# Optimization experiments

Hardware: AMD Instinct MI355X
Metric: run time of the kernel (lower is better)

The kernel has to match this reference:

```python
import math
import jax, jax.numpy as jnp
import numpy as np

L, H, C, T = 6, 16, 1024, 256   # layers, heads, n_embd, context steps (seq = 3T)
NACT, D_FF, B = 80, 4096, 4

def _conv(x, w, b, s, p):
    y = jax.lax.conv_general_dilated(x, w, (s, s), [(p, p), (p, p)],
                                     dimension_numbers=('NCHW', 'OIHW', 'NCHW'))
    return y + b[None, :, None, None]

def _ln(x, g, b):
    m = x.mean(-1, keepdims=True)
    v = ((x - m) ** 2).mean(-1, keepdims=True)
    return (x - m) / jnp.sqrt(v + 1e-5) * g + b

def _forward(states, rtgs, meta_states, circuit_feas,
             conv1_w, conv1_b, conv2_w, conv2_b, conv3_w, conv3_b,
             enc_w, enc_b, meta_w1, meta_b1, meta_w2, meta_b2,
             ret_w, ret_b, act_emb, pos_emb, gpos_emb,
             ln1_g, ln1_b, ln2_g, ln2_b,
             Wq, bq, Wk, bk, Wv, bv, Wo, bo,
             Wm1, bm1, Wm2, bm2, lnf_g, lnf_b, head_w,
             actions, timesteps):
    Bb, Tl = states.shape[0], states.shape[1]
    # state CNN encoder: (B*T, 8, 8, 10) -> 16 feats -> Linear(16, C-4)
    s = states.reshape(-1, 8, 8, 10)
    h = jax.nn.relu(_conv(s, conv1_w, conv1_b, 2, 1))
    h = jax.nn.relu(_conv(h, conv2_w, conv2_b, 2, 1))
    h = jax.nn.relu(_conv(h, conv3_w, conv3_b, 2, 1))
    se = h.reshape(h.shape[0], -1) @ enc_w + enc_b                    # (B*T, C-4)
    me = jax.nn.relu(meta_states.reshape(-1, 4) @ meta_w1 + meta_b1) @ meta_w2 + meta_b2
    state_emb = jnp.tanh(jnp.concatenate([se, me], axis=1)).reshape(Bb, Tl, C)
    # circuit embedding is computed then zeroed in source (no_circuit_emb=True) -> no effect
    rtg_emb = jnp.tanh(rtgs @ ret_w + ret_b)                          # (B, T, C)
    act_e = act_emb[actions[..., 0]]                                  # (B, T, C)
    # interleave (rtg, state, action) per timestep -> (B, 3T, C)
    tok = jnp.stack([rtg_emb, state_emb, act_e], axis=2).reshape(Bb, 3 * Tl, C)
    pos = gpos_emb[0, timesteps[:, 0, 0]][:, None, :] + pos_emb[:, :3 * Tl, :]
    x = tok + pos
    mask = jnp.tril(jnp.ones((3 * Tl, 3 * Tl), bool))
    d = C // H
    for i in range(L):
        hx = _ln(x, ln1_g[i], ln1_b[i])
        q = (hx @ Wq[i] + bq[i]).reshape(Bb, 3 * Tl, H, d)
        k = (hx @ Wk[i] + bk[i]).reshape(Bb, 3 * Tl, H, d)
        v = (hx @ Wv[i] + bv[i]).reshape(Bb, 3 * Tl, H, d)
        att = jnp.einsum('bqhd,bkhd->bhqk', q, k) / math.sqrt(d)
        att = jax.nn.softmax(jnp.where(mask, att, -jnp.inf), axis=-1)
        y = jnp.einsum('bhqk,bkhd->bqhd', att, v).reshape(Bb, 3 * Tl, C)
        x = x + (y @ Wo[i] + bo[i])
        h2 = _ln(x, ln2_g[i], ln2_b[i])
        x = x + (jax.nn.gelu(h2 @ Wm1[i] + bm1[i], approximate=False) @ Wm2[i] + bm2[i])
    logits = _ln(x, lnf_g, lnf_b) @ head_w                            # (B, 3T, NACT)
    return logits[:, 1::3, :]                                         # predictions at state tokens

def setup_inputs():
    ks = iter(jax.random.split(jax.random.key(0), 64))
    def W(*shape):
        return jax.random.normal(next(ks), shape, jnp.float32) * 0.02
    return {
        'states': jax.random.normal(next(ks), (B, T, 640), jnp.float32),
        'rtgs': jax.random.normal(next(ks), (B, T, 1), jnp.float32),
        'meta_states': jax.random.normal(next(ks), (B, T, 4), jnp.float32),
        'circuit_feas': jax.random.normal(next(ks), (B, 768), jnp.float32),
        'conv1_w': W(16, 8, 8, 8), 'conv1_b': jnp.zeros(16),
        'conv2_w': W(32, 16, 4, 4), 'conv2_b': jnp.zeros(32),
        'conv3_w': W(16, 32, 3, 3), 'conv3_b': jnp.zeros(16),
        'enc_w': W(16, C - 4), 'enc_b': jnp.zeros(C - 4),
        'meta_w1': W(4, 32), 'meta_b1': jnp.zeros(32),
        'meta_w2': W(32, 4), 'meta_b2': jnp.zeros(4),
        'ret_w': W(1, C), 'ret_b': jnp.zeros(C),
        'act_emb': W(NACT, C),
        'pos_emb': W(1, 3 * T + 1, C), 'gpos_emb': W(1, T + 1, C),
        'ln1_g': jnp.ones((L, C)), 'ln1_b': jnp.zeros((L, C)),
        'ln2_g': jnp.ones((L, C)), 'ln2_b': jnp.zeros((L, C)),
        'Wq': W(L, C, C), 'bq': jnp.zeros((L, C)),
        'Wk': W(L, C, C), 'bk': jnp.zeros((L, C)),
        'Wv': W(L, C, C), 'bv': jnp.zeros((L, C)),
        'Wo': W(L, C, C), 'bo': jnp.zeros((L, C)),
        'Wm1': W(L, C, D_FF), 'bm1': jnp.zeros((L, D_FF)),
        'Wm2': W(L, D_FF, C), 'bm2': jnp.zeros((L, C)),
        'lnf_g': jnp.ones(C), 'lnf_b': jnp.zeros(C),
        'head_w': W(C, NACT),
        'actions': jax.random.randint(next(ks), (B, T, 1), 0, NACT),
        'timesteps': jax.random.randint(next(ks), (B, 1, 1), 0, T + 1),
    }

def reference(states, rtgs, meta_states, circuit_feas,
              conv1_w, conv1_b, conv2_w, conv2_b, conv3_w, conv3_b,
              enc_w, enc_b, meta_w1, meta_b1, meta_w2, meta_b2,
              ret_w, ret_b, act_emb, pos_emb, gpos_emb,
              ln1_g, ln1_b, ln2_g, ln2_b,
              Wq, bq, Wk, bk, Wv, bv, Wo, bo,
              Wm1, bm1, Wm2, bm2, lnf_g, lnf_b, head_w,
              actions, timesteps):
    return _forward(states, rtgs, meta_states, circuit_feas,
                    conv1_w, conv1_b, conv2_w, conv2_b, conv3_w, conv3_b,
                    enc_w, enc_b, meta_w1, meta_b1, meta_w2, meta_b2,
                    ret_w, ret_b, act_emb, pos_emb, gpos_emb,
                    ln1_g, ln1_b, ln2_g, ln2_b,
                    Wq, bq, Wk, bk, Wv, bv, Wo, bo,
                    Wm1, bm1, Wm2, bm2, lnf_g, lnf_b, head_w,
                    actions, timesteps)
```

## Files before the change

### kernel.cpp

```cpp
#include <hip/hip_runtime.h>
#include <hip/hip_bf16.h>


#define S_LEN 768
#define C_DIM 1024
#define NHEAD 16
#define HDIM 64
#define BATCH 4
#define TCTX 256
#define DFF 4096
#define NACT 80
#define MROWS (BATCH * S_LEN)

typedef __attribute__((ext_vector_type(4))) float f32x4;
typedef __attribute__((ext_vector_type(8))) short bf16x8;
typedef __attribute__((ext_vector_type(8))) _Float16 f16x8;

static __device__ __forceinline__ unsigned short f2bf(float f) {
    unsigned int u = __float_as_uint(f);
    u += 0x7FFF + ((u >> 16) & 1);
    return (unsigned short)(u >> 16);
}
static __device__ __forceinline__ float bf2f(unsigned short h) {
    return __uint_as_float(((unsigned int)h) << 16);
}
static __device__ __forceinline__ unsigned short f2h(float f) {
    _Float16 h = (_Float16)f;
    return __builtin_bit_cast(unsigned short, h);
}

static __device__ __forceinline__ void gload16(void* l, const void* g) {
    __builtin_amdgcn_global_load_lds(
        (__attribute__((address_space(1))) void*)(g),
        (__attribute__((address_space(3))) void*)(l), 16, 0, 0);
}

__global__ __launch_bounds__(256) void transpose_w_kernel(
    const float* __restrict__ Wq, const float* __restrict__ Wk,
    const float* __restrict__ Wv, const float* __restrict__ Wo,
    const float* __restrict__ Wm1, const float* __restrict__ Wm2,
    unsigned short* __restrict__ Wb)
{
    const int t = blockIdx.x;
    const float* src; unsigned short* dst; int K, N, kt, nt;
    if (t < 1024) {
        const int m = t >> 8, tile = t & 255;
        src = (m == 0) ? Wq : (m == 1) ? Wk : (m == 2) ? Wv : Wo;
        dst = Wb + (size_t)m * 1048576;
        K = 1024; N = 1024; kt = tile >> 4; nt = tile & 15;
    } else if (t < 2048) {
        const int tile = t - 1024;
        src = Wm1; dst = Wb + (size_t)4 * 1048576;
        K = 1024; N = 4096; kt = tile >> 6; nt = tile & 63;
    } else {
        const int tile = t - 2048;
        src = Wm2; dst = Wb + (size_t)8 * 1048576;
        K = 4096; N = 1024; kt = tile >> 4; nt = tile & 15;
    }
    const int k0 = kt * 64, n0 = nt * 64;
    __shared__ float Ls[64][65];

    const int r = threadIdx.x >> 2, p = threadIdx.x & 3;
    #pragma unroll
    for (int i = 0; i < 4; ++i)
        *(float4*)&Ls[r][p * 16 + i * 4] =
            *(const float4*)&src[(size_t)(k0 + r) * N + n0 + p * 16 + i * 4];
    __syncthreads();

    unsigned short __align__(16) h[16];
    #pragma unroll
    for (int i = 0; i < 16; ++i) h[i] = f2bf(Ls[p * 16 + i][r]);
    unsigned short* d = dst + (size_t)(n0 + r) * K + k0 + p * 16;
    *(uint4*)d       = *(uint4*)&h[0];
    *(uint4*)(d + 8) = *(uint4*)&h[8];
}

__global__ __launch_bounds__(256) void embed_kernel(
    const float* __restrict__ states, const float* __restrict__ rtgs,
    const float* __restrict__ meta,
    const float* __restrict__ c1w, const float* __restrict__ c1b,
    const float* __restrict__ c2w, const float* __restrict__ c2b,
    const float* __restrict__ c3w, const float* __restrict__ c3b,
    const float* __restrict__ encw, const float* __restrict__ encb,
    const float* __restrict__ mw1, const float* __restrict__ mb1,
    const float* __restrict__ mw2, const float* __restrict__ mb2,
    const float* __restrict__ retw, const float* __restrict__ retb,
    const float* __restrict__ aemb, const float* __restrict__ pos,
    const float* __restrict__ gpos,
    const int* __restrict__ actions, const int* __restrict__ timesteps,
    float* __restrict__ X)
{
    const int n = blockIdx.x;
    const int b = n >> 8, t = n & 255;
    const int tid = threadIdx.x;

    __shared__ float sin_[640];
    __shared__ float h1[96];
    __shared__ float h2[32];
    __shared__ float feat[16];
    __shared__ float hidm[32];
    __shared__ float mer[4];

    for (int e = tid; e < 640; e += 256)
        sin_[e] = states[(size_t)n * 640 + e];
    __syncthreads();

    if (tid < 96) {
        int o = tid / 6, rem = tid % 6, oh = rem / 3, ow = rem % 3;
        float a = c1b[o];
        for (int ci = 0; ci < 8; ++ci)
            for (int kh = 0; kh < 8; ++kh) {
                int ih = oh * 2 - 1 + kh;
                if (ih < 0 || ih >= 8) continue;
                for (int kw = 0; kw < 8; ++kw) {
                    int iw = ow * 2 - 1 + kw;
                    if (iw < 0 || iw >= 10) continue;
                    a += c1w[((o * 8 + ci) * 8 + kh) * 8 + kw] * sin_[ci * 80 + ih * 10 + iw];
                }
            }
        h1[tid] = fmaxf(a, 0.f);
    }
    if (tid < 32) {
        float a = mb1[tid];
        for (int i = 0; i < 4; ++i)
            a += meta[(size_t)n * 4 + i] * mw1[i * 32 + tid];
        hidm[tid] = fmaxf(a, 0.f);
    }
    __syncthreads();

    if (tid < 32) {
        float a = c2b[tid];
        for (int ci = 0; ci < 16; ++ci)
            for (int kh = 0; kh < 4; ++kh) {
                int ih = -1 + kh;
                if (ih < 0 || ih >= 2) continue;
                for (int kw = 0; kw < 4; ++kw) {
                    int iw = -1 + kw;
                    if (iw < 0 || iw >= 3) continue;
                    a += c2w[((tid * 16 + ci) * 4 + kh) * 4 + kw] * h1[ci * 6 + ih * 3 + iw];
                }
            }
        h2[tid] = fmaxf(a, 0.f);
    }
    __syncthreads();

    if (tid < 16) {
        float a = c3b[tid];
        for (int ci = 0; ci < 32; ++ci)
            a += c3w[(tid * 32 + ci) * 9 + 4] * h2[ci];
        feat[tid] = fmaxf(a, 0.f);
    }
    if (tid < 4) {
        float a = mb2[tid];
        for (int j = 0; j < 32; ++j) a += hidm[j] * mw2[j * 4 + tid];
        mer[tid] = a;
    }
    __syncthreads();

    const float r = rtgs[n];
    const int a_idx = actions[n];
    const int g = timesteps[b];
    const size_t xbase = ((size_t)b * S_LEN + 3 * t) * C_DIM;

    for (int c = tid; c < C_DIM; c += 256) {
        float se;
        if (c < 1020) {
            float acc = encb[c];
            #pragma unroll
            for (int k = 0; k < 16; ++k) acc += feat[k] * encw[k * 1020 + c];
            se = acc;
        } else {
            se = mer[c - 1020];
        }
        const float st = tanhf(se);
        const float rt = tanhf(r * retw[c] + retb[c]);
        const float ae = aemb[(size_t)a_idx * C_DIM + c];
        const float gp = gpos[(size_t)g * C_DIM + c];
        X[xbase + c]             = rt + gp + pos[(size_t)(3 * t + 0) * C_DIM + c];
        X[xbase + C_DIM + c]     = st + gp + pos[(size_t)(3 * t + 1) * C_DIM + c];
        X[xbase + 2 * C_DIM + c] = ae + gp + pos[(size_t)(3 * t + 2) * C_DIM + c];
    }
}

__global__ __launch_bounds__(256) void ln_bf16_kernel(
    const float* __restrict__ in, unsigned short* __restrict__ out,
    const float* __restrict__ gw, const float* __restrict__ bw)
{
    const int row = blockIdx.x * 4 + (threadIdx.x >> 6);
    const int lane = threadIdx.x & 63;
    const float* x = in + (size_t)row * C_DIM;

    float4 v[4];
    float s = 0.f;
    #pragma unroll
    for (int j = 0; j < 4; ++j) {
        v[j] = *(const float4*)&x[lane * 4 + j * 256];
        s += (v[j].x + v[j].y) + (v[j].z + v[j].w);
    }
    #pragma unroll
    for (int o = 1; o < 64; o <<= 1) s += __shfl_xor(s, o, 64);
    const float mean = s * (1.0f / 1024.0f);

    float s2 = 0.f;
    #pragma unroll
    for (int j = 0; j < 4; ++j) {
        float dx = v[j].x - mean, dy = v[j].y - mean;
        float dz = v[j].z - mean, dw = v[j].w - mean;
        s2 += (dx * dx + dy * dy) + (dz * dz + dw * dw);
    }
    #pragma unroll
    for (int o = 1; o < 64; o <<= 1) s2 += __shfl_xor(s2, o, 64);
    const float inv = rsqrtf(s2 * (1.0f / 1024.0f) + 1e-5f);

    #pragma unroll
    for (int j = 0; j < 4; ++j) {
        const int c = lane * 4 + j * 256;
        ushort4 o4;
        o4.x = f2bf((v[j].x - mean) * inv * gw[c + 0] + bw[c + 0]);
        o4.y = f2bf((v[j].y - mean) * inv * gw[c + 1] + bw[c + 1]);
        o4.z = f2bf((v[j].z - mean) * inv * gw[c + 2] + bw[c + 2]);
        o4.w = f2bf((v[j].w - mean) * inv * gw[c + 3] + bw[c + 3]);
        *(ushort4*)&out[(size_t)row * C_DIM + c] = o4;
    }
}

__device__ __forceinline__ void gemm_core(
    const unsigned short* __restrict__ A, const unsigned short* __restrict__ Bt,
    int row0, int col0, int ldk, int nk, f32x4 (&acc)[4][4])
{
    __shared__ __align__(16) unsigned short As[3][4][128][8];
    __shared__ __align__(16) unsigned short Bs[3][4][128][8];

    const int tid = threadIdx.x;
    const int ar  = tid & 63, akg = tid >> 6;
    const int lane = tid & 63, w = tid >> 6;
    const int rwl = (w >> 1) * 64, cwl = (w & 1) * 64;
    const int mi = lane & 15, kg = lane >> 4;

    const unsigned short* pa = A + (size_t)(row0 + ar) * ldk + akg * 8;
    const unsigned short* pb = Bt + (size_t)(col0 + ar) * ldk + akg * 8;
    const size_t rstep = (size_t)64 * ldk;

    gload16(&As[0][akg][ar][0],      pa);
    gload16(&As[0][akg][ar + 64][0], pa + rstep);
    gload16(&Bs[0][akg][ar][0],      pb);
    gload16(&Bs[0][akg][ar + 64][0], pb + rstep);
    gload16(&As[1][akg][ar][0],      pa + 32);
    gload16(&As[1][akg][ar + 64][0], pa + rstep + 32);
    gload16(&Bs[1][akg][ar][0],      pb + 32);
    gload16(&Bs[1][akg][ar + 64][0], pb + rstep + 32);

#define GEMM_STEP(CB, PB, KK, VM)                                          \
    {                                                                      \
        asm volatile("s_waitcnt vmcnt(" #VM ")" ::: "memory");             \
        __builtin_amdgcn_s_barrier();                                      \
        __builtin_amdgcn_sched_barrier(0);                                 \
        if ((KK) + 2 < nk) {                                               \
            const unsigned short* ga = pa + (size_t)((KK) + 2) * 32;       \
            const unsigned short* gb = pb + (size_t)((KK) + 2) * 32;       \
            gload16(&As[PB][akg][ar][0],      ga);                         \
            gload16(&As[PB][akg][ar + 64][0], ga + rstep);                 \
            gload16(&Bs[PB][akg][ar][0],      gb);                         \
            gload16(&Bs[PB][akg][ar + 64][0], gb + rstep);                 \
        }                                                                  \
        bf16x8 af[4], bfr[4];                                              \
        _Pragma("unroll")                                                  \
        for (int i = 0; i < 4; ++i) {                                      \
            af[i]  = *(const bf16x8*)&As[CB][kg][rwl + i * 16 + mi][0];    \
            bfr[i] = *(const bf16x8*)&Bs[CB][kg][cwl + i * 16 + mi][0];    \
        }                                                                  \
        __builtin_amdgcn_s_setprio(1);                                     \
        _Pragma("unroll")                                                  \
        for (int ri = 0; ri < 4; ++ri)                                     \
            _Pragma("unroll")                                              \
            for (int ci = 0; ci < 4; ++ci)                                 \
                acc[ri][ci] = __builtin_amdgcn_mfma_f32_16x16x32_bf16(     \
                    af[ri], bfr[ci], acc[ri][ci], 0, 0, 0);                \
        __builtin_amdgcn_s_setprio(0);                                     \
    }

    int k = 0;
    while (k + 4 < nk) {
        GEMM_STEP(0, 2, k,     4)
        GEMM_STEP(1, 0, k + 1, 4)
        GEMM_STEP(2, 1, k + 2, 4)
        k += 3;
    }
    GEMM_STEP(0, 2, k,     4)
    GEMM_STEP(1, 0, k + 1, 0)
#undef GEMM_STEP
}

template<int ACT, int OUTB, int RES>
__global__ __launch_bounds__(256) void mfma_gemm(
    const unsigned short* __restrict__ A, const unsigned short* __restrict__ Bt,
    const float* __restrict__ bias, const float* resid,
    float* outf, unsigned short* __restrict__ outb,
    int N, int K)
{
    const int row0 = blockIdx.y * 128, col0 = blockIdx.x * 128;
    f32x4 acc[4][4] = {};
    gemm_core(A, Bt, row0, col0, K, K >> 5, acc);

    const int lane = threadIdx.x & 63, w = threadIdx.x >> 6;
    const int rwl = (w >> 1) * 64, cwl = (w & 1) * 64;
    const int mi = lane & 15, kg = lane >> 4;

    #pragma unroll
    for (int ri = 0; ri < 4; ++ri) {
        #pragma unroll
        for (int ci = 0; ci < 4; ++ci) {
            #pragma unroll
            for (int j = 0; j < 4; ++j) {
                const int row = row0 + rwl + ri * 16 + kg * 4 + j;
                const int col = col0 + cwl + ci * 16 + mi;
                float v = acc[ri][ci][j] + bias[col];
                if (ACT) v = 0.5f * v * (1.0f + erff(v * 0.70710678118f));
                if (RES) v += resid[(size_t)row * N + col];
                if (OUTB) outb[(size_t)row * N + col] = f2bf(v);
                else      outf[(size_t)row * N + col] = v;
            }
        }
    }
}

__global__ __launch_bounds__(256) void mfma_gemm_ressplit(
    const unsigned short* __restrict__ A, const unsigned short* __restrict__ Bt,
    const float* __restrict__ bias, float* __restrict__ X,
    int N, int K)
{
    const int row0 = blockIdx.y * 128, col0 = blockIdx.x * 128;
    const int ks = blockIdx.z;
    const int kseg = K >> 2;
    f32x4 acc[4][4] = {};
    gemm_core(A + (size_t)ks * kseg, Bt + (size_t)ks * kseg,
              row0, col0, K, kseg >> 5, acc);

    const int lane = threadIdx.x & 63, w = threadIdx.x >> 6;
    const int rwl = (w >> 1) * 64, cwl = (w & 1) * 64;
    const int mi = lane & 15, kg = lane >> 4;

    #pragma unroll
    for (int ri = 0; ri < 4; ++ri)
        #pragma unroll
        for (int ci = 0; ci < 4; ++ci)
            #pragma unroll
            for (int j = 0; j < 4; ++j) {
                const int row = row0 + rwl + ri * 16 + kg * 4 + j;
                const int col = col0 + cwl + ci * 16 + mi;
                float v = acc[ri][ci][j] + (ks == 0 ? bias[col] : 0.f);
                atomicAdd(&X[(size_t)row * N + col], v);
            }
}

__global__ __launch_bounds__(256) void mfma_gemm_qk(
    const unsigned short* __restrict__ A, const unsigned short* __restrict__ Wb,
    const float* __restrict__ bq, const float* __restrict__ bk,
    unsigned short* __restrict__ Qh, unsigned short* __restrict__ Kh)
{
    const int grp = blockIdx.x >> 3;
    const unsigned short* Bt = Wb + (size_t)grp * 1048576;
    const float* bias = grp == 0 ? bq : bk;
    unsigned short* out = grp == 0 ? Qh : Kh;
    const float scale = grp == 0 ? 0.125f : 1.0f;
    const int row0 = blockIdx.y * 128, col0 = (blockIdx.x & 7) * 128;

    f32x4 acc[4][4] = {};
    gemm_core(A, Bt, row0, col0, C_DIM, 32, acc);

    const int lane = threadIdx.x & 63, w = threadIdx.x >> 6;
    const int rwl = (w >> 1) * 64, cwl = (w & 1) * 64;
    const int mi = lane & 15, kg = lane >> 4;

    #pragma unroll
    for (int ri = 0; ri < 4; ++ri)
        #pragma unroll
        for (int ci = 0; ci < 4; ++ci)
            #pragma unroll
            for (int j = 0; j < 4; ++j) {
                const int row = row0 + rwl + ri * 16 + kg * 4 + j;
                const int col = col0 + cwl + ci * 16 + mi;
                out[(size_t)row * C_DIM + col] = f2h((acc[ri][ci][j] + bias[col]) * scale);
            }
}

__global__ __launch_bounds__(256) void mfma_gemm_vt(
    const unsigned short* __restrict__ WvT, const unsigned short* __restrict__ Xb,
    const float* __restrict__ bv, unsigned short* __restrict__ Vt)
{
    const int row0 = blockIdx.y * 128, col0 = blockIdx.x * 128;
    f32x4 acc[4][4] = {};
    gemm_core(WvT, Xb, row0, col0, C_DIM, 32, acc);

    const int lane = threadIdx.x & 63, w = threadIdx.x >> 6;
    const int rwl = (w >> 1) * 64, cwl = (w & 1) * 64;
    const int mi = lane & 15, kg = lane >> 4;

    #pragma unroll
    for (int ri = 0; ri < 4; ++ri)
        #pragma unroll
        for (int ci = 0; ci < 4; ++ci)
            #pragma unroll
            for (int j = 0; j < 4; ++j) {
                const int row = row0 + rwl + ri * 16 + kg * 4 + j;
                const int col = col0 + cwl + ci * 16 + mi;
                Vt[(size_t)row * MROWS + col] = f2h(acc[ri][ci][j] + bv[row]);
            }
}

__global__ __launch_bounds__(256) void attn_mfma(
    const unsigned short* __restrict__ Qh, const unsigned short* __restrict__ Kh,
    const unsigned short* __restrict__ Vt, unsigned short* __restrict__ Yb)
{
    const int qt = blockIdx.x, h = blockIdx.y, b = blockIdx.z;
    const int tid = threadIdx.x;
    const int lane = tid & 63, w = tid >> 6;
    const int mi = lane & 15, kg = lane >> 4;
    const int q0 = qt * 64;

    __shared__ __align__(16) char ldsraw[24576];
    unsigned short* Ks = (unsigned short*)ldsraw;
    unsigned short* Vs = (unsigned short*)(ldsraw + 8192);
    unsigned short* Ps = (unsigned short*)(ldsraw + 16384);
    float* Ob = (float*)ldsraw;

    const size_t qkbase = (size_t)b * S_LEN * C_DIM + (size_t)h * HDIM;
    const unsigned short* Kbase = Kh + qkbase;
    const unsigned short* Vbase = Vt + (size_t)h * HDIM * MROWS + (size_t)b * S_LEN;

    f16x8 QA0, QA1;
    {
        const unsigned short* qp = Qh + qkbase + (size_t)(q0 + w * 16 + mi) * C_DIM + kg * 8;
        QA0 = *(const f16x8*)qp;
        QA1 = *(const f16x8*)(qp + 32);
    }

    const int srow = tid >> 3, sc16 = tid & 7;
    const int dch = (sc16 ^ (srow & 7)) << 3;

    float mrow[4], lrow[4], alj[4];
    f32x4 Oacc[4];
    #pragma unroll
    for (int j = 0; j < 4; ++j) { mrow[j] = -1e30f; lrow[j] = 0.f; }
    #pragma unroll
    for (int df = 0; df < 4; ++df) Oacc[df] = (f32x4){0.f, 0.f, 0.f, 0.f};

    uint4 rk0, rk1, rv0, rv1;
    {
        const unsigned short* kp = Kbase + (size_t)srow * C_DIM + sc16 * 8;
        rk0 = *(const uint4*)kp;
        rk1 = *(const uint4*)(kp + (size_t)32 * C_DIM);
        const unsigned short* vp = Vbase + (size_t)srow * MROWS + sc16 * 8;
        rv0 = *(const uint4*)vp;
        rv1 = *(const uint4*)(vp + (size_t)32 * MROWS);
    }

    for (int kt = 0; kt <= qt; ++kt) {
        __syncthreads();
        *(uint4*)&Ks[srow * 64 + dch]        = rk0;
        *(uint4*)&Ks[(srow + 32) * 64 + dch] = rk1;
        *(uint4*)&Vs[srow * 64 + dch]        = rv0;
        *(uint4*)&Vs[(srow + 32) * 64 + dch] = rv1;
        if (kt < qt) {
            const unsigned short* kp = Kbase + (size_t)((kt + 1) * 64 + srow) * C_DIM + sc16 * 8;
            rk0 = *(const uint4*)kp;
            rk1 = *(const uint4*)(kp + (size_t)32 * C_DIM);
            const unsigned short* vp = Vbase + (size_t)srow * MROWS + (kt + 1) * 64 + sc16 * 8;
            rv0 = *(const uint4*)vp;
            rv1 = *(const uint4*)(vp + (size_t)32 * MROWS);
        }
        __syncthreads();

        f32x4 sa[4];
        #pragma unroll
        for (int kf = 0; kf < 4; ++kf) {
            const int key = kf * 16 + mi;
            const unsigned short* kr = Ks + key * 64;
            const f16x8 kb0 = *(const f16x8*)(kr + ((kg ^ (key & 7)) << 3));
            const f16x8 kb1 = *(const f16x8*)(kr + (((4 + kg) ^ (key & 7)) << 3));
            f32x4 z = {0.f, 0.f, 0.f, 0.f};
            z = __builtin_amdgcn_mfma_f32_16x16x32_f16(QA0, kb0, z, 0, 0, 0);
            sa[kf] = __builtin_amdgcn_mfma_f32_16x16x32_f16(QA1, kb1, z, 0, 0, 0);
        }

        if (kt == qt) {
            #pragma unroll
            for (int kf = 0; kf < 4; ++kf)
                #pragma unroll
                for (int j = 0; j < 4; ++j)
                    if (kf * 16 + mi > w * 16 + kg * 4 + j) sa[kf][j] = -1e30f;
        }

        #pragma unroll
        for (int j = 0; j < 4; ++j) {
            float rm = fmaxf(fmaxf(sa[0][j], sa[1][j]), fmaxf(sa[2][j], sa[3][j]));
            rm = fmaxf(rm, __shfl_xor(rm, 1, 16));
            rm = fmaxf(rm, __shfl_xor(rm, 2, 16));
            rm = fmaxf(rm, __shfl_xor(rm, 4, 16));
            rm = fmaxf(rm, __shfl_xor(rm, 8, 16));
            const float mn = fmaxf(mrow[j], rm);
            alj[j] = __expf(mrow[j] - mn);
            mrow[j] = mn;
            const float p0 = __expf(sa[0][j] - mn);
            const float p1 = __expf(sa[1][j] - mn);
            const float p2 = __expf(sa[2][j] - mn);
            const float p3 = __expf(sa[3][j] - mn);
            const int prow = w * 16 + kg * 4 + j;
            unsigned short* pr = Ps + prow * 64;
            const int sw = prow & 7, hi = mi >> 3, lo = mi & 7;
            pr[(((0 + hi) ^ sw) << 3) + lo] = f2h(p0);
            pr[(((2 + hi) ^ sw) << 3) + lo] = f2h(p1);
            pr[(((4 + hi) ^ sw) << 3) + lo] = f2h(p2);
            pr[(((6 + hi) ^ sw) << 3) + lo] = f2h(p3);
            float rs = p0 + p1 + p2 + p3;
            rs += __shfl_xor(rs, 1, 16);
            rs += __shfl_xor(rs, 2, 16);
            rs += __shfl_xor(rs, 4, 16);
            rs += __shfl_xor(rs, 8, 16);
            lrow[j] = lrow[j] * alj[j] + rs;
        }

        const unsigned short* pp = Ps + (w * 16 + mi) * 64;
        const int psw = mi & 7;
        const f16x8 PA0 = *(const f16x8*)(pp + ((kg ^ psw) << 3));
        const f16x8 PA1 = *(const f16x8*)(pp + (((4 + kg) ^ psw) << 3));
        #pragma unroll
        for (int df = 0; df < 4; ++df) {
            const int d = df * 16 + mi;
            const unsigned short* vr = Vs + d * 64;
            const f16x8 vb0 = *(const f16x8*)(vr + ((kg ^ (d & 7)) << 3));
            const f16x8 vb1 = *(const f16x8*)(vr + (((4 + kg) ^ (d & 7)) << 3));
            f32x4 o = Oacc[df];
            o[0] *= alj[0]; o[1] *= alj[1]; o[2] *= alj[2]; o[3] *= alj[3];
            o = __builtin_amdgcn_mfma_f32_16x16x32_f16(PA0, vb0, o, 0, 0, 0);
            Oacc[df] = __builtin_amdgcn_mfma_f32_16x16x32_f16(PA1, vb1, o, 0, 0, 0);
        }
    }

    __syncthreads();
    float inv[4];
    #pragma unroll
    for (int j = 0; j < 4; ++j) inv[j] = 1.0f / lrow[j];
    #pragma unroll
    for (int df = 0; df < 4; ++df)
        #pragma unroll
        for (int j = 0; j < 4; ++j)
            Ob[(w * 16 + kg * 4 + j) * 68 + df * 16 + mi] = Oacc[df][j] * inv[j];
    __syncthreads();

    const int orow = tid >> 2, oc0 = (tid & 3) * 16;
    unsigned short __align__(16) hx[16];
    #pragma unroll
    for (int i = 0; i < 16; ++i) hx[i] = f2bf(Ob[orow * 68 + oc0 + i]);
    unsigned short* yp = Yb + qkbase + (size_t)(q0 + orow) * C_DIM + oc0;
    *(uint4*)yp       = *(uint4*)&hx[0];
    *(uint4*)(yp + 8) = *(uint4*)&hx[8];
}

__global__ __launch_bounds__(256) void head_kernel(
    const unsigned short* __restrict__ Xb, const float* __restrict__ hw,
    float* __restrict__ out)
{
    const int n = blockIdx.x;
    const int b = n >> 8, t = n & 255;
    const int tid = threadIdx.x;
    __shared__ float rowv[C_DIM];

    const unsigned short* x = Xb + ((size_t)b * S_LEN + 3 * t + 1) * C_DIM;
    #pragma unroll
    for (int j = 0; j < 4; ++j) rowv[tid + j * 256] = bf2f(x[tid + j * 256]);
    __syncthreads();

    if (tid < NACT) {
        float a = 0.f;
        for (int k = 0; k < C_DIM; ++k) a += rowv[k] * hw[k * NACT + tid];
        out[(size_t)n * NACT + tid] = a;
    }
}

extern "C" void kernel_launch(void* const* d_in, const int* in_sizes, int n_in,
                              void* d_out, int out_size, void* d_ws, size_t ws_size,
                              hipStream_t stream) {
    const float* states  = (const float*)d_in[0];
    const float* rtgs    = (const float*)d_in[1];
    const float* meta    = (const float*)d_in[2];
    const float* c1w = (const float*)d_in[4];
    const float* c1b = (const float*)d_in[5];
    const float* c2w = (const float*)d_in[6];
    const float* c2b = (const float*)d_in[7];
    const float* c3w = (const float*)d_in[8];
    const float* c3b = (const float*)d_in[9];
    const float* encw = (const float*)d_in[10];
    const float* encb = (const float*)d_in[11];
    const float* mw1 = (const float*)d_in[12];
    const float* mb1 = (const float*)d_in[13];
    const float* mw2 = (const float*)d_in[14];
    const float* mb2 = (const float*)d_in[15];
    const float* retw = (const float*)d_in[16];
    const float* retb = (const float*)d_in[17];
    const float* aemb = (const float*)d_in[18];
    const float* pos  = (const float*)d_in[19];
    const float* gpos = (const float*)d_in[20];
    const float* ln1g = (const float*)d_in[21];
    const float* ln1b = (const float*)d_in[22];
    const float* ln2g = (const float*)d_in[23];
    const float* ln2b = (const float*)d_in[24];
    const float* Wq = (const float*)d_in[25];
    const float* bq = (const float*)d_in[26];
    const float* Wk = (const float*)d_in[27];
    const float* bk = (const float*)d_in[28];
    const float* Wv = (const float*)d_in[29];
    const float* bv = (const float*)d_in[30];
    const float* Wo = (const float*)d_in[31];
    const float* bo = (const float*)d_in[32];
    const float* Wm1 = (const float*)d_in[33];
    const float* bm1 = (const float*)d_in[34];
    const float* Wm2 = (const float*)d_in[35];
    const float* bm2 = (const float*)d_in[36];
    const float* lnfg = (const float*)d_in[37];
    const float* lnfb = (const float*)d_in[38];
    const float* hw   = (const float*)d_in[39];
    const int* actions   = (const int*)d_in[40];
    const int* timesteps = (const int*)d_in[41];

    float* out = (float*)d_out;

    char* wsc = (char*)d_ws;
    const size_t SLABB = (size_t)MROWS * C_DIM * 4;
    float* X  = (float*)wsc;
    unsigned short* Qh = (unsigned short*)(wsc + SLABB);
    unsigned short* Kh = Qh + (size_t)MROWS * C_DIM;
    unsigned short* Vt = (unsigned short*)(wsc + 2 * SLABB);
    unsigned short* Hb = (unsigned short*)(wsc + SLABB);
    unsigned short* Xb = (unsigned short*)(wsc + 4 * SLABB);
    unsigned short* Yb = (unsigned short*)(wsc + 4 * SLABB + SLABB / 2);
    unsigned short* Wb = (unsigned short*)(wsc + 5 * SLABB);

    embed_kernel<<<BATCH * TCTX, 256, 0, stream>>>(
        states, rtgs, meta, c1w, c1b, c2w, c2b, c3w, c3b, encw, encb,
        mw1, mb1, mw2, mb2, retw, retb, aemb, pos, gpos, actions, timesteps, X);

    const dim3 gqk(16, 24);
    const dim3 gvt(24, 8);
    const dim3 gres(8, 24, 4);
    const dim3 g4096(32, 24);
    const dim3 gattn(12, NHEAD, BATCH);

    for (int i = 0; i < 6; ++i) {
        const size_t wOff = (size_t)i * C_DIM * C_DIM;
        const size_t bOff = (size_t)i * C_DIM;
        const size_t m1Off = (size_t)i * C_DIM * DFF;

        transpose_w_kernel<<<3072, 256, 0, stream>>>(
            Wq + wOff, Wk + wOff, Wv + wOff, Wo + wOff, Wm1 + m1Off, Wm2 + m1Off, Wb);

        ln_bf16_kernel<<<MROWS / 4, 256, 0, stream>>>(X, Xb, ln1g + bOff, ln1b + bOff);
        mfma_gemm_qk<<<gqk, 256, 0, stream>>>(Xb, Wb, bq + bOff, bk + bOff, Qh, Kh);
        mfma_gemm_vt<<<gvt, 256, 0, stream>>>(Wb + (size_t)2 * 1048576, Xb, bv + bOff, Vt);
        attn_mfma<<<gattn, 256, 0, stream>>>(Qh, Kh, Vt, Yb);
        mfma_gemm_ressplit<<<gres, 256, 0, stream>>>(
            Yb, Wb + (size_t)3 * 1048576, bo + bOff, X, C_DIM, C_DIM);
        ln_bf16_kernel<<<MROWS / 4, 256, 0, stream>>>(X, Xb, ln2g + bOff, ln2b + bOff);
        mfma_gemm<1, 1, 0><<<g4096, 256, 0, stream>>>(
            Xb, Wb + (size_t)4 * 1048576, bm1 + (size_t)i * DFF, nullptr, nullptr, Hb, DFF, C_DIM);
        mfma_gemm_ressplit<<<gres, 256, 0, stream>>>(
            Hb, Wb + (size_t)8 * 1048576, bm2 + bOff, X, C_DIM, DFF);
    }

    ln_bf16_kernel<<<MROWS / 4, 256, 0, stream>>>(X, Xb, lnfg, lnfb);
    head_kernel<<<BATCH * TCTX, 256, 0, stream>>>(Xb, hw, out);
}
```

Before: 2.459 ms.

## Swizzle block indices for XCD-local reuse and fuse QK and V-transpose GEMMs

Remaps the linear block index in the MLP-up, residual split-K and attention kernels so blocks sharing the same A rows or head land on the same XCD (block id mod 8), improving L2 reuse on MI355X's chiplet layout. Attention also issues the longest causal query tiles first. The separate QK and V-transpose GEMM launches are merged into a single 576-block launch, which removes one launch and fills the GPU better. The risk is that the index mapping assumes round-robin XCD dispatch, and a wrong decode would leave tiles missing.

```diff
diff --git a/kernel.cpp b/kernel.cpp
--- a/kernel.cpp
+++ b/kernel.cpp
@@ -291,14 +291,16 @@
 #undef GEMM_STEP
 }
 
-template<int ACT, int OUTB, int RES>
-__global__ __launch_bounds__(256) void mfma_gemm(
+__global__ __launch_bounds__(256) void mfma_gemm_up(
     const unsigned short* __restrict__ A, const unsigned short* __restrict__ Bt,
-    const float* __restrict__ bias, const float* resid,
-    float* outf, unsigned short* __restrict__ outb,
+    const float* __restrict__ bias, unsigned short* __restrict__ outb,
     int N, int K)
 {
-    const int row0 = blockIdx.y * 128, col0 = blockIdx.x * 128;
+    const int h = blockIdx.x + (blockIdx.y << 5);
+    const int xcd = h & 7, s = h >> 3;
+    const int col0 = (s & 31) * 128;
+    const int row0 = (xcd + 8 * (s >> 5)) * 128;
+
     f32x4 acc[4][4] = {};
     gemm_core(A, Bt, row0, col0, K, K >> 5, acc);
 
@@ -307,21 +309,17 @@
     const int mi = lane & 15, kg = lane >> 4;
 
     #pragma unroll
-    for (int ri = 0; ri < 4; ++ri) {
-        #pragma unroll
-        for (int ci = 0; ci < 4; ++ci) {
+    for (int ri = 0; ri < 4; ++ri)
+        #pragma unroll
+        for (int ci = 0; ci < 4; ++ci)
             #pragma unroll
             for (int j = 0; j < 4; ++j) {
                 const int row = row0 + rwl + ri * 16 + kg * 4 + j;
                 const int col = col0 + cwl + ci * 16 + mi;
                 float v = acc[ri][ci][j] + bias[col];
-                if (ACT) v = 0.5f * v * (1.0f + erff(v * 0.70710678118f));
-                if (RES) v += resid[(size_t)row * N + col];
-                if (OUTB) outb[(size_t)row * N + col] = f2bf(v);
-                else      outf[(size_t)row * N + col] = v;
+                v = 0.5f * v * (1.0f + erff(v * 0.70710678118f));
+                outb[(size_t)row * N + col] = f2bf(v);
             }
-        }
-    }
 }
 
 __global__ __launch_bounds__(256) void mfma_gemm_ressplit(
@@ -329,8 +327,12 @@
     const float* __restrict__ bias, float* __restrict__ X,
     int N, int K)
 {
-    const int row0 = blockIdx.y * 128, col0 = blockIdx.x * 128;
-    const int ks = blockIdx.z;
+    const int h = blockIdx.x + (blockIdx.y << 3) + blockIdx.z * 192;
+    const int xcd = h & 7, s = h >> 3;
+    const int ks = s & 3;
+    const int col0 = ((s >> 2) & 7) * 128;
+    const int row0 = (xcd + 8 * (s >> 5)) * 128;
+
     const int kseg = K >> 2;
     f32x4 acc[4][4] = {};
     gemm_core(A + (size_t)ks * kseg, Bt + (size_t)ks * kseg,
@@ -353,17 +355,31 @@
             }
 }
 
-__global__ __launch_bounds__(256) void mfma_gemm_qk(
-    const unsigned short* __restrict__ A, const unsigned short* __restrict__ Wb,
+__global__ __launch_bounds__(256) void mfma_gemm_qkvt(
+    const unsigned short* __restrict__ Xb, const unsigned short* __restrict__ Wb,
     const float* __restrict__ bq, const float* __restrict__ bk,
-    unsigned short* __restrict__ Qh, unsigned short* __restrict__ Kh)
-{
-    const int grp = blockIdx.x >> 3;
-    const unsigned short* Bt = Wb + (size_t)grp * 1048576;
-    const float* bias = grp == 0 ? bq : bk;
-    unsigned short* out = grp == 0 ? Qh : Kh;
-    const float scale = grp == 0 ? 0.125f : 1.0f;
-    const int row0 = blockIdx.y * 128, col0 = (blockIdx.x & 7) * 128;
+    const float* __restrict__ bv,
+    unsigned short* __restrict__ Qh, unsigned short* __restrict__ Kh,
+    unsigned short* __restrict__ Vt)
+{
+    const int h = blockIdx.x;
+    const unsigned short *A, *Bt;
+    int row0, col0, grp = -1;
+
+    if (h < 384) {
+        const int xcd = h & 7, s = h >> 3;
+        const int x = s & 15;
+        const int y = xcd + 8 * (s >> 4);
+        grp = x >> 3;
+        A = Xb; Bt = Wb + (size_t)grp * 1048576;
+        row0 = y * 128; col0 = (x & 7) * 128;
+    } else {
+        const int j = h - 384;
+        const int xcd = j & 7, s = j >> 3;
+        A = Wb + (size_t)2 * 1048576; Bt = Xb;
+        row0 = xcd * 128;
+        col0 = s * 128;
+    }
 
     f32x4 acc[4][4] = {};
     gemm_core(A, Bt, row0, col0, C_DIM, 32, acc);
@@ -372,47 +388,45 @@
     const int rwl = (w >> 1) * 64, cwl = (w & 1) * 64;
     const int mi = lane & 15, kg = lane >> 4;
 
-    #pragma unroll
-    for (int ri = 0; ri < 4; ++ri)
-        #pragma unroll
-        for (int ci = 0; ci < 4; ++ci)
+    if (grp >= 0) {
+        const float* bias = grp == 0 ? bq : bk;
+        unsigned short* out = grp == 0 ? Qh : Kh;
+        const float scale = grp == 0 ? 0.125f : 1.0f;
+        #pragma unroll
+        for (int ri = 0; ri < 4; ++ri)
             #pragma unroll
-            for (int j = 0; j < 4; ++j) {
-                const int row = row0 + rwl + ri * 16 + kg * 4 + j;
-                const int col = col0 + cwl + ci * 16 + mi;
-                out[(size_t)row * C_DIM + col] = f2h((acc[ri][ci][j] + bias[col]) * scale);
-            }
-}
-
-__global__ __launch_bounds__(256) void mfma_gemm_vt(
-    const unsigned short* __restrict__ WvT, const unsigned short* __restrict__ Xb,
-    const float* __restrict__ bv, unsigned short* __restrict__ Vt)
-{
-    const int row0 = blockIdx.y * 128, col0 = blockIdx.x * 128;
-    f32x4 acc[4][4] = {};
-    gemm_core(WvT, Xb, row0, col0, C_DIM, 32, acc);
-
-    const int lane = threadIdx.x & 63, w = threadIdx.x >> 6;
-    const int rwl = (w >> 1) * 64, cwl = (w & 1) * 64;
-    const int mi = lane & 15, kg = lane >> 4;
-
-    #pragma unroll
-    for (int ri = 0; ri < 4; ++ri)
-        #pragma unroll
-        for (int ci = 0; ci < 4; ++ci)
+            for (int ci = 0; ci < 4; ++ci)
+                #pragma unroll
+                for (int j = 0; j < 4; ++j) {
+                    const int row = row0 + rwl + ri * 16 + kg * 4 + j;
+                    const int col = col0 + cwl + ci * 16 + mi;
+                    out[(size_t)row * C_DIM + col] =
+                        f2h((acc[ri][ci][j] + bias[col]) * scale);
+                }
+    } else {
+        #pragma unroll
+        for (int ri = 0; ri < 4; ++ri)
             #pragma unroll
-            for (int j = 0; j < 4; ++j) {
-                const int row = row0 + rwl + ri * 16 + kg * 4 + j;
-                const int col = col0 + cwl + ci * 16 + mi;
-                Vt[(size_t)row * MROWS + col] = f2h(acc[ri][ci][j] + bv[row]);
-            }
+            for (int ci = 0; ci < 4; ++ci)
+                #pragma unroll
+                for (int j = 0; j < 4; ++j) {
+                    const int row = row0 + rwl + ri * 16 + kg * 4 + j;
+                    const int col = col0 + cwl + ci * 16 + mi;
+                    Vt[(size_t)row * MROWS + col] = f2h(acc[ri][ci][j] + bv[row]);
+                }
+    }
 }
 
 __global__ __launch_bounds__(256) void attn_mfma(
     const unsigned short* __restrict__ Qh, const unsigned short* __restrict__ Kh,
     const unsigned short* __restrict__ Vt, unsigned short* __restrict__ Yb)
 {
-    const int qt = blockIdx.x, h = blockIdx.y, b = blockIdx.z;
+    const int hw = blockIdx.x + 12 * (blockIdx.y + 16 * blockIdx.z);
+    const int xcd = hw & 7, s = hw >> 3;
+    const int qt = 11 - (s % 12);
+    const int pair = xcd + 8 * (s / 12);
+    const int h = pair & 15, b = pair >> 4;
+
     const int tid = threadIdx.x;
     const int lane = tid & 63, w = tid >> 6;
     const int mi = lane & 15, kg = lane >> 4;
@@ -640,8 +654,6 @@
         states, rtgs, meta, c1w, c1b, c2w, c2b, c3w, c3b, encw, encb,
         mw1, mb1, mw2, mb2, retw, retb, aemb, pos, gpos, actions, timesteps, X);
 
-    const dim3 gqk(16, 24);
-    const dim3 gvt(24, 8);
     const dim3 gres(8, 24, 4);
     const dim3 g4096(32, 24);
     const dim3 gattn(12, NHEAD, BATCH);
@@ -655,14 +667,14 @@
             Wq + wOff, Wk + wOff, Wv + wOff, Wo + wOff, Wm1 + m1Off, Wm2 + m1Off, Wb);
 
         ln_bf16_kernel<<<MROWS / 4, 256, 0, stream>>>(X, Xb, ln1g + bOff, ln1b + bOff);
-        mfma_gemm_qk<<<gqk, 256, 0, stream>>>(Xb, Wb, bq + bOff, bk + bOff, Qh, Kh);
-        mfma_gemm_vt<<<gvt, 256, 0, stream>>>(Wb + (size_t)2 * 1048576, Xb, bv + bOff, Vt);
+        mfma_gemm_qkvt<<<576, 256, 0, stream>>>(
+            Xb, Wb, bq + bOff, bk + bOff, bv + bOff, Qh, Kh, Vt);
         attn_mfma<<<gattn, 256, 0, stream>>>(Qh, Kh, Vt, Yb);
         mfma_gemm_ressplit<<<gres, 256, 0, stream>>>(
             Yb, Wb + (size_t)3 * 1048576, bo + bOff, X, C_DIM, C_DIM);
         ln_bf16_kernel<<<MROWS / 4, 256, 0, stream>>>(X, Xb, ln2g + bOff, ln2b + bOff);
-        mfma_gemm<1, 1, 0><<<g4096, 256, 0, stream>>>(
-            Xb, Wb + (size_t)4 * 1048576, bm1 + (size_t)i * DFF, nullptr, nullptr, Hb, DFF, C_DIM);
+        mfma_gemm_up<<<g4096, 256, 0, stream>>>(
+            Xb, Wb + (size_t)4 * 1048576, bm1 + (size_t)i * DFF, Hb, DFF, C_DIM);
         mfma_gemm_ressplit<<<gres, 256, 0, stream>>>(
             Hb, Wb + (size_t)8 * 1048576, bm2 + bOff, X, C_DIM, DFF);
     }
```

Measured after the change: 2.415 ms. Within noise of the previous version (-1.8%).
